# Optimization experiments

Hardware: AMD Instinct MI355X
Metric: run time of the kernel (lower is better)

## Reference

```python
import jax, jax.numpy as jnp
import numpy as np

HID, H, D, DFF = 128, 4, 128, 2048   # hidden_dim, nheads, out_feats per head, dim_feedforward
N, E, B = 32768, 524288, 32
EPS = 1e-5
SLOPE = 0.2  # DGL EdgeGATConv negative_slope default


def setup_inputs() -> dict:
    key = jax.random.key(0)
    ks = jax.random.split(key, 16)
    s = 0.05
    return {
        "h": jax.random.normal(ks[0], (N, HID), jnp.float32),
        "e": jax.random.normal(ks[1], (E, 1), jnp.float32),
        "src": jax.random.randint(ks[2], (E,), 0, N, jnp.int32),
        "dst": jax.random.randint(ks[3], (E,), 0, N, jnp.int32),
        "batch_size": B,
        # EdgeGATConv params (fc / fc_edge / res_fc are bias-free in DGL)
        "W_fc": jax.random.normal(ks[4], (HID, H * D), jnp.float32) * s,
        "attn_l": jax.random.normal(ks[5], (H, D), jnp.float32) * s,
        "attn_r": jax.random.normal(ks[6], (H, D), jnp.float32) * s,
        "W_fe": jax.random.normal(ks[7], (1, H * D), jnp.float32) * s,
        "attn_e": jax.random.normal(ks[8], (H, D), jnp.float32) * s,
        "W_res": jax.random.normal(ks[9], (HID, H * D), jnp.float32) * s,
        "gat_bias": jnp.zeros((H * D,), jnp.float32),
        # linear_mha + norms + FFN
        "W_mha": jax.random.normal(ks[10], (H * D, HID), jnp.float32) * s,
        "b_mha": jnp.zeros((HID,), jnp.float32),
        "n1_g": jnp.ones((HID,), jnp.float32),
        "n1_b": jnp.zeros((HID,), jnp.float32),
        "n2_g": jnp.ones((HID,), jnp.float32),
        "n2_b": jnp.zeros((HID,), jnp.float32),
        "W1": jax.random.normal(ks[11], (HID, DFF), jnp.float32) * s,
        "b1": jnp.zeros((DFF,), jnp.float32),
        "W2": jax.random.normal(ks[12], (DFF, HID), jnp.float32) * s,
        "b2": jnp.zeros((HID,), jnp.float32),
    }


def _ln(x, g, b):
    mu = x.mean(-1, keepdims=True)
    var = ((x - mu) ** 2).mean(-1, keepdims=True)
    return (x - mu) * jax.lax.rsqrt(var + EPS) * g + b


def reference(h, e, src, dst, batch_size, W_fc, attn_l, attn_r, W_fe, attn_e,
              W_res, gat_bias, W_mha, b_mha, n1_g, n1_b, n2_g, n2_b,
              W1, b1, W2, b2):
    n = h.shape[0]
    h0 = h
    # --- EdgeGATConv (eval mode: dropouts are identity) ---
    ft = (h @ W_fc).reshape(n, H, D)                         # (N,H,D)
    el = jnp.einsum("nhd,hd->nh", ft, attn_l)                # (N,H)
    er = jnp.einsum("nhd,hd->nh", ft, attn_r)
    fe = (e @ W_fe).reshape(-1, H, D)                        # (E,H,D)
    ee = jnp.einsum("ehd,hd->eh", fe, attn_e)                # (E,H)
    sc = jax.nn.leaky_relu(el[src] + er[dst] + ee, SLOPE)    # (E,H)
    # segment softmax over incoming edges of each dst node
    m = jax.ops.segment_max(sc, dst, num_segments=n)         # (N,H)
    m = jnp.where(jnp.isfinite(m), m, 0.0)                   # empty segments
    w = jnp.exp(sc - m[dst])
    z = jax.ops.segment_sum(w, dst, num_segments=n)
    zd = z[dst]
    alpha = w / jnp.where(zd == 0, 1.0, zd)                  # (E,H)
    msg = ft[src] * alpha[:, :, None]                        # (E,H,D)
    rst = jax.ops.segment_sum(msg, dst, num_segments=n)      # (N,H,D)
    rst = rst + (h0 @ W_res).reshape(n, H, D) + gat_bias.reshape(1, H, D)
    # --- transformer wrapper ---
    x = jax.nn.relu(rst).reshape(n, H * D)
    x = jax.nn.relu(x @ W_mha + b_mha)
    x = _ln(h0 + x, n1_g, n1_b)
    x = x.reshape(batch_size, -1, x.shape[1])                # (B, N/B, HID)
    ff = jax.nn.relu(x @ W1 + b1) @ W2 + b2
    return _ln(x + ff, n2_g, n2_b)
```

## Files before the change

kernel.cpp:

```cpp
#include <hip/hip_runtime.h>
#include <hip/hip_bf16.h>

#define N_NODES 32768
#define E_EDGES 524288
#define HIDDIM 128
#define FDIM 512
#define DFF 2048
#define LN_EPS 1e-5f
#define SLOPE 0.2f
#define CAP 64

typedef __bf16 bf16_t;
typedef __bf16 bf16x8 __attribute__((ext_vector_type(8)));
typedef float f32x4 __attribute__((ext_vector_type(4)));
typedef float f32x2 __attribute__((ext_vector_type(2)));

#define GLD_LDS16(gp, lp) __builtin_amdgcn_global_load_lds( \
    (const __attribute__((address_space(1))) unsigned int*)(gp), \
    (__attribute__((address_space(3))) unsigned int*)(lp), 16, 0, 0)

__device__ inline unsigned char f32_to_e4m3(float v) {
#if __has_builtin(__builtin_amdgcn_cvt_pk_fp8_f32)
    return (unsigned char)(__builtin_amdgcn_cvt_pk_fp8_f32(v, v, 0, false) & 0xff);
#else
    unsigned bits = __float_as_uint(v);
    unsigned sign = (bits >> 24) & 0x80;
    float av = fabsf(v);
    if (av >= 448.f) return (unsigned char)(sign | 0x7E);
    int e = (int)((bits >> 23) & 0xFF) - 127;
    if (e < -6) { int n = (int)rintf(av * 512.f); return (unsigned char)(sign | n); }
    float ulp = exp2f((float)(e - 3));
    int n = (int)rintf(av / ulp);
    if (n == 16) { e += 1; n = 8; }
    return (unsigned char)(sign | ((e + 7) << 3) | (n - 8));
#endif
}
template<bool HI>
__device__ inline f32x2 e4m3x2_to_f32(unsigned u) {
#if __has_builtin(__builtin_amdgcn_cvt_pk_f32_fp8)
    return __builtin_amdgcn_cvt_pk_f32_fp8(u, HI);
#else
    f32x2 r;
    unsigned b0 = HI ? ((u >> 16) & 0xff) : (u & 0xff);
    unsigned b1 = HI ? ((u >> 24) & 0xff) : ((u >> 8) & 0xff);
    unsigned bs[2] = {b0, b1};
    for (int i = 0; i < 2; ++i) {
        unsigned b = bs[i];
        float s = (b & 0x80) ? -1.f : 1.f;
        int e = (b >> 3) & 15, m = b & 7;
        float v = e ? (8 + m) * exp2f((float)(e - 10)) : m * exp2f(-9.f);
        r[i] = s * v;
    }
    return r;
#endif
}

__global__ __launch_bounds__(256) void gemm_mfma(const bf16_t* __restrict__ A,
                                                 const bf16_t* __restrict__ Bp,
                                                 bf16_t* __restrict__ C,
                                                 int M, int N, int K) {
    __shared__ __align__(16) bf16_t lA[4096];
    __shared__ __align__(16) bf16_t lB[4096];
    const int tid = threadIdx.x;
    const int lane = tid & 63;
    const int wave = tid >> 6;
    const int wm = (wave >> 1) * 64, wn = (wave & 1) * 64;
    const int row0 = blockIdx.y * 128, col0 = blockIdx.x * 128;
    const int ko = lane >> 4;
    const int rl = lane & 15;
    f32x4 acc[4][4] = {};
    const int c0 = tid, c1 = tid + 256;
    const int g0 = c0 >> 7, m0 = c0 & 127;
    const int g1 = c1 >> 7, m1 = c1 & 127;
    for (int k0 = 0; k0 < K; k0 += 32) {
        __syncthreads();
        GLD_LDS16(A + (size_t)(row0 + m0) * K + k0 + g0 * 8, lA + c0 * 8);
        GLD_LDS16(A + (size_t)(row0 + m1) * K + k0 + g1 * 8, lA + c1 * 8);
        GLD_LDS16(Bp + ((size_t)(k0 / 8 + g0) * N + col0 + m0) * 8, lB + c0 * 8);
        GLD_LDS16(Bp + ((size_t)(k0 / 8 + g1) * N + col0 + m1) * 8, lB + c1 * 8);
        __syncthreads();
        bf16x8 af[4], bfr[4];
#pragma unroll
        for (int i = 0; i < 4; ++i) {
            af[i]  = *(const bf16x8*)&lA[(ko * 128 + wm + i * 16 + rl) * 8];
            bfr[i] = *(const bf16x8*)&lB[(ko * 128 + wn + i * 16 + rl) * 8];
        }
#pragma unroll
        for (int i = 0; i < 4; ++i)
#pragma unroll
            for (int j = 0; j < 4; ++j)
                acc[i][j] = __builtin_amdgcn_mfma_f32_16x16x32_bf16(af[i], bfr[j], acc[i][j], 0, 0, 0);
    }
    const int cr = (lane >> 4) * 4;
    const int cc = lane & 15;
#pragma unroll
    for (int i = 0; i < 4; ++i)
#pragma unroll
        for (int j = 0; j < 4; ++j) {
            const int col = col0 + wn + j * 16 + cc;
#pragma unroll
            for (int r = 0; r < 4; ++r) {
                const int row = row0 + wm + i * 16 + cr + r;
                C[(size_t)row * N + col] = (bf16_t)acc[i][j][r];
            }
        }
}

__global__ __launch_bounds__(256) void gemm_ft(const bf16_t* __restrict__ A,
                                               const bf16_t* __restrict__ Bp,
                                               const float* __restrict__ attn_l,
                                               const float* __restrict__ attn_r,
                                               unsigned char* __restrict__ ft8,
                                               float* __restrict__ el,
                                               float* __restrict__ er) {
    __shared__ __align__(16) bf16_t lA[4096];
    __shared__ __align__(16) bf16_t lB[4096];
    __shared__ float s_el[2][128], s_er[2][128];
    const int tid = threadIdx.x, lane = tid & 63, wave = tid >> 6;
    const int wm = (wave >> 1) * 64, wn = (wave & 1) * 64;
    const int row0 = blockIdx.y * 128;
    const int head = blockIdx.x, col0 = head * 128;
    const int ko = lane >> 4, rl = lane & 15;
    f32x4 acc[4][4] = {};
    const int c0 = tid, c1 = tid + 256;
    const int g0 = c0 >> 7, m0 = c0 & 127;
    const int g1 = c1 >> 7, m1 = c1 & 127;
    for (int k0 = 0; k0 < 128; k0 += 32) {
        __syncthreads();
        GLD_LDS16(A + (size_t)(row0 + m0) * 128 + k0 + g0 * 8, lA + c0 * 8);
        GLD_LDS16(A + (size_t)(row0 + m1) * 128 + k0 + g1 * 8, lA + c1 * 8);
        GLD_LDS16(Bp + ((size_t)(k0 / 8 + g0) * 512 + col0 + m0) * 8, lB + c0 * 8);
        GLD_LDS16(Bp + ((size_t)(k0 / 8 + g1) * 512 + col0 + m1) * 8, lB + c1 * 8);
        __syncthreads();
        bf16x8 af[4], bfr[4];
#pragma unroll
        for (int i = 0; i < 4; ++i) {
            af[i]  = *(const bf16x8*)&lA[(ko * 128 + wm + i * 16 + rl) * 8];
            bfr[i] = *(const bf16x8*)&lB[(ko * 128 + wn + i * 16 + rl) * 8];
        }
#pragma unroll
        for (int i = 0; i < 4; ++i)
#pragma unroll
            for (int j = 0; j < 4; ++j)
                acc[i][j] = __builtin_amdgcn_mfma_f32_16x16x32_bf16(af[i], bfr[j], acc[i][j], 0, 0, 0);
    }
    const int cr = (lane >> 4) * 4, cc = lane & 15;
    float al[4], ar[4];
#pragma unroll
    for (int j = 0; j < 4; ++j) {
        al[j] = attn_l[col0 + wn + j * 16 + cc];
        ar[j] = attn_r[col0 + wn + j * 16 + cc];
    }
#pragma unroll
    for (int i = 0; i < 4; ++i)
#pragma unroll
        for (int r = 0; r < 4; ++r) {
            const int row = row0 + wm + i * 16 + cr + r;
            float pel = 0.f, per = 0.f;
#pragma unroll
            for (int j = 0; j < 4; ++j) {
                const float v = acc[i][j][r];
                ft8[(size_t)row * 512 + col0 + wn + j * 16 + cc] = f32_to_e4m3(v);
                pel += v * al[j];
                per += v * ar[j];
            }
#pragma unroll
            for (int m = 1; m < 16; m <<= 1) {
                pel += __shfl_xor(pel, m);
                per += __shfl_xor(per, m);
            }
            if (cc == 0) {
                s_el[wn >> 6][wm + i * 16 + cr + r] = pel;
                s_er[wn >> 6][wm + i * 16 + cr + r] = per;
            }
        }
    __syncthreads();
    if (tid < 128) {
        el[(size_t)(row0 + tid) * 4 + head] = s_el[0][tid] + s_el[1][tid];
        er[(size_t)(row0 + tid) * 4 + head] = s_er[0][tid] + s_er[1][tid];
    }
}

__global__ __launch_bounds__(256) void gemm_mha_ln(const bf16_t* __restrict__ A,
                                                   const bf16_t* __restrict__ Bp,
                                                   const float* __restrict__ bias,
                                                   const float* __restrict__ h0,
                                                   const float* __restrict__ gamma,
                                                   const float* __restrict__ beta,
                                                   bf16_t* __restrict__ out) {
    __shared__ __align__(16) bf16_t lA[4096];
    __shared__ __align__(16) bf16_t lB[4096];
    __shared__ float s_s1[2][128], s_s2[2][128], s_mu[128], s_rs[128];
    const int tid = threadIdx.x, lane = tid & 63, wave = tid >> 6;
    const int wm = (wave >> 1) * 64, wn = (wave & 1) * 64;
    const int row0 = blockIdx.x * 128;
    const int ko = lane >> 4, rl = lane & 15;
    f32x4 acc[4][4] = {};
    const int c0 = tid, c1 = tid + 256;
    const int g0 = c0 >> 7, m0 = c0 & 127;
    const int g1 = c1 >> 7, m1 = c1 & 127;
    for (int k0 = 0; k0 < 512; k0 += 32) {
        __syncthreads();
        GLD_LDS16(A + (size_t)(row0 + m0) * 512 + k0 + g0 * 8, lA + c0 * 8);
        GLD_LDS16(A + (size_t)(row0 + m1) * 512 + k0 + g1 * 8, lA + c1 * 8);
        GLD_LDS16(Bp + ((size_t)(k0 / 8 + g0) * 128 + m0) * 8, lB + c0 * 8);
        GLD_LDS16(Bp + ((size_t)(k0 / 8 + g1) * 128 + m1) * 8, lB + c1 * 8);
        __syncthreads();
        bf16x8 af[4], bfr[4];
#pragma unroll
        for (int i = 0; i < 4; ++i) {
            af[i]  = *(const bf16x8*)&lA[(ko * 128 + wm + i * 16 + rl) * 8];
            bfr[i] = *(const bf16x8*)&lB[(ko * 128 + wn + i * 16 + rl) * 8];
        }
#pragma unroll
        for (int i = 0; i < 4; ++i)
#pragma unroll
            for (int j = 0; j < 4; ++j)
                acc[i][j] = __builtin_amdgcn_mfma_f32_16x16x32_bf16(af[i], bfr[j], acc[i][j], 0, 0, 0);
    }
    const int cr = (lane >> 4) * 4, cc = lane & 15;
#pragma unroll
    for (int j = 0; j < 4; ++j) {
        const int col = wn + j * 16 + cc;
        const float bb = bias[col];
#pragma unroll
        for (int i = 0; i < 4; ++i)
#pragma unroll
            for (int r = 0; r < 4; ++r) {
                const int row = row0 + wm + i * 16 + cr + r;
                acc[i][j][r] = fmaxf(acc[i][j][r] + bb, 0.f) + h0[(size_t)row * 128 + col];
            }
    }
#pragma unroll
    for (int i = 0; i < 4; ++i)
#pragma unroll
        for (int r = 0; r < 4; ++r) {
            float s1 = 0.f, s2 = 0.f;
#pragma unroll
            for (int j = 0; j < 4; ++j) { const float v = acc[i][j][r]; s1 += v; s2 += v * v; }
#pragma unroll
            for (int m = 1; m < 16; m <<= 1) {
                s1 += __shfl_xor(s1, m);
                s2 += __shfl_xor(s2, m);
            }
            if (cc == 0) {
                s_s1[wn >> 6][wm + i * 16 + cr + r] = s1;
                s_s2[wn >> 6][wm + i * 16 + cr + r] = s2;
            }
        }
    __syncthreads();
    if (tid < 128) {
        const float a = s_s1[0][tid] + s_s1[1][tid];
        const float q = s_s2[0][tid] + s_s2[1][tid];
        const float mu = a * (1.f / 128.f);
        s_mu[tid] = mu;
        s_rs[tid] = rsqrtf(q * (1.f / 128.f) - mu * mu + LN_EPS);
    }
    __syncthreads();
#pragma unroll
    for (int j = 0; j < 4; ++j) {
        const int col = wn + j * 16 + cc;
        const float gg = gamma[col], bb = beta[col];
#pragma unroll
        for (int i = 0; i < 4; ++i)
#pragma unroll
            for (int r = 0; r < 4; ++r) {
                const int rloc = wm + i * 16 + cr + r;
                out[(size_t)(row0 + rloc) * 128 + col] =
                    (bf16_t)((acc[i][j][r] - s_mu[rloc]) * s_rs[rloc] * gg + bb);
            }
    }
}

__global__ __launch_bounds__(256, 1) void ffn_fused(const bf16_t* __restrict__ x3,
                                                    const bf16_t* __restrict__ W1p,
                                                    const float* __restrict__ b1,
                                                    const bf16_t* __restrict__ W2p,
                                                    const float* __restrict__ b2,
                                                    const float* __restrict__ gamma,
                                                    const float* __restrict__ beta,
                                                    float* __restrict__ out) {
    __shared__ __align__(16) bf16_t lX[16384];
    __shared__ __align__(16) bf16_t lW1[16384];
    __shared__ __align__(16) bf16_t lW2[16384];
    __shared__ __align__(16) bf16_t lY[16384];
    __shared__ float s_s1[2][128], s_s2[2][128], s_mu[128], s_rs[128];
    const int tid = threadIdx.x, lane = tid & 63, wave = tid >> 6;
    const int wm = (wave >> 1) * 64, wn = (wave & 1) * 64;
    const int row0 = blockIdx.x * 128;
    const int ko = lane >> 4, rl = lane & 15;
    const int cr = (lane >> 4) * 4, cc = lane & 15;
#pragma unroll
    for (int it = 0; it < 8; ++it) {
        const int c = it * 256 + tid;
        const int g = c >> 7, m = c & 127;
        GLD_LDS16(x3 + (size_t)(row0 + m) * 128 + g * 8, lX + c * 8);
    }
    f32x4 xacc[4][4] = {};
    for (int ch = 0; ch < 16; ++ch) {
        __syncthreads();
#pragma unroll
        for (int it = 0; it < 8; ++it) {
            const int c = it * 256 + tid;
            const int g = c >> 7, n = c & 127;
            GLD_LDS16(W1p + ((size_t)g * 2048 + ch * 128 + n) * 8, lW1 + c * 8);
            GLD_LDS16(W2p + ((size_t)(ch * 16 + g) * 128 + n) * 8, lW2 + c * 8);
        }
        __syncthreads();
        f32x4 yacc[4][4] = {};
#pragma unroll
        for (int kk = 0; kk < 4; ++kk) {
            bf16x8 af[4], bfr[4];
#pragma unroll
            for (int i = 0; i < 4; ++i) {
                af[i]  = *(const bf16x8*)&lX[((kk * 4 + ko) * 128 + wm + i * 16 + rl) * 8];
                bfr[i] = *(const bf16x8*)&lW1[((kk * 4 + ko) * 128 + wn + i * 16 + rl) * 8];
            }
#pragma unroll
            for (int i = 0; i < 4; ++i)
#pragma unroll
                for (int j = 0; j < 4; ++j)
                    yacc[i][j] = __builtin_amdgcn_mfma_f32_16x16x32_bf16(af[i], bfr[j], yacc[i][j], 0, 0, 0);
        }
#pragma unroll
        for (int j = 0; j < 4; ++j) {
            const int col = wn + j * 16 + cc;
            const float bb = b1[ch * 128 + col];
#pragma unroll
            for (int i = 0; i < 4; ++i)
#pragma unroll
                for (int r = 0; r < 4; ++r) {
                    const float v = fmaxf(yacc[i][j][r] + bb, 0.f);
                    const int row = wm + i * 16 + cr + r;
                    lY[((col >> 3) * 128 + row) * 8 + (col & 7)] = (bf16_t)v;
                }
        }
        __syncthreads();
#pragma unroll
        for (int kk = 0; kk < 4; ++kk) {
            bf16x8 af[4], bfr[4];
#pragma unroll
            for (int i = 0; i < 4; ++i) {
                af[i]  = *(const bf16x8*)&lY[((kk * 4 + ko) * 128 + wm + i * 16 + rl) * 8];
                bfr[i] = *(const bf16x8*)&lW2[((kk * 4 + ko) * 128 + wn + i * 16 + rl) * 8];
            }
#pragma unroll
            for (int i = 0; i < 4; ++i)
#pragma unroll
                for (int j = 0; j < 4; ++j)
                    xacc[i][j] = __builtin_amdgcn_mfma_f32_16x16x32_bf16(af[i], bfr[j], xacc[i][j], 0, 0, 0);
        }
    }
#pragma unroll
    for (int j = 0; j < 4; ++j) {
        const int col = wn + j * 16 + cc;
        const float bb = b2[col];
#pragma unroll
        for (int i = 0; i < 4; ++i)
#pragma unroll
            for (int r = 0; r < 4; ++r) {
                const int row = wm + i * 16 + cr + r;
                const float x3v = (float)lX[((col >> 3) * 128 + row) * 8 + (col & 7)];
                xacc[i][j][r] += bb + x3v;
            }
    }
#pragma unroll
    for (int i = 0; i < 4; ++i)
#pragma unroll
        for (int r = 0; r < 4; ++r) {
            float s1 = 0.f, s2 = 0.f;
#pragma unroll
            for (int j = 0; j < 4; ++j) { const float v = xacc[i][j][r]; s1 += v; s2 += v * v; }
#pragma unroll
            for (int m = 1; m < 16; m <<= 1) {
                s1 += __shfl_xor(s1, m);
                s2 += __shfl_xor(s2, m);
            }
            if (cc == 0) {
                s_s1[wn >> 6][wm + i * 16 + cr + r] = s1;
                s_s2[wn >> 6][wm + i * 16 + cr + r] = s2;
            }
        }
    __syncthreads();
    if (tid < 128) {
        const float a = s_s1[0][tid] + s_s1[1][tid];
        const float q = s_s2[0][tid] + s_s2[1][tid];
        const float mu = a * (1.f / 128.f);
        s_mu[tid] = mu;
        s_rs[tid] = rsqrtf(q * (1.f / 128.f) - mu * mu + LN_EPS);
    }
    __syncthreads();
#pragma unroll
    for (int j = 0; j < 4; ++j) {
        const int col = wn + j * 16 + cc;
        const float gg = gamma[col], bb = beta[col];
#pragma unroll
        for (int i = 0; i < 4; ++i)
#pragma unroll
            for (int r = 0; r < 4; ++r) {
                const int rloc = wm + i * 16 + cr + r;
                out[(size_t)(row0 + rloc) * 128 + col] =
                    (xacc[i][j][r] - s_mu[rloc]) * s_rs[rloc] * gg + bb;
            }
    }
}

__global__ __launch_bounds__(256) void pack_b(const float* __restrict__ B, bf16_t* __restrict__ out,
                                              int K8, int N) {
    const int id = blockIdx.x * 256 + threadIdx.x;
    if (id >= K8 * N) return;
    const int g = id / N, n = id % N;
    union { bf16_t b[8]; uint4 u; } pk;
#pragma unroll
    for (int j = 0; j < 8; ++j) pk.b[j] = (bf16_t)B[(size_t)(g * 8 + j) * N + n];
    *(uint4*)(out + (size_t)id * 8) = pk.u;
}

__global__ __launch_bounds__(256) void f2b_kernel(const float* __restrict__ x, bf16_t* __restrict__ o) {
    const int id = blockIdx.x * 256 + threadIdx.x;
    const float4 v = ((const float4*)x)[id];
    union { bf16_t b[4]; uint2 u; } pk;
    pk.b[0] = (bf16_t)v.x; pk.b[1] = (bf16_t)v.y; pk.b[2] = (bf16_t)v.z; pk.b[3] = (bf16_t)v.w;
    *(uint2*)(o + (size_t)id * 4) = pk.u;
}

__global__ __launch_bounds__(128) void ce_kernel(const float* __restrict__ W_fe,
                                                 const float* __restrict__ attn_e,
                                                 float* __restrict__ ce) {
    const int t = threadIdx.x;
    const float4 w = ((const float4*)W_fe)[t];
    const float4 a = ((const float4*)attn_e)[t];
    float p = w.x * a.x + w.y * a.y + w.z * a.z + w.w * a.w;
    for (int off = 16; off; off >>= 1) p += __shfl_down(p, off, 32);
    if ((t & 31) == 0) ce[t >> 5] = p;
}

__global__ __launch_bounds__(256) void edge_build(const float* __restrict__ evals,
                                                  const int* __restrict__ src,
                                                  const int* __restrict__ dst,
                                                  const float* __restrict__ el,
                                                  const float* __restrict__ er,
                                                  const float* __restrict__ ce,
                                                  int* __restrict__ cursor,
                                                  int* __restrict__ csr_src,
                                                  float4* __restrict__ csr_w) {
    const int e = blockIdx.x * 256 + threadIdx.x;
    const int s = src[e], d = dst[e];
    const float ev = evals[e];
    const float4 l = *(const float4*)(el + (size_t)s * 4);
    const float4 r = *(const float4*)(er + (size_t)d * 4);
    const float4 c = *(const float4*)ce;
    float4 w;
    {
        float v;
        v = l.x + r.x + ev * c.x; v = v >= 0.f ? v : SLOPE * v; w.x = expf(v);
        v = l.y + r.y + ev * c.y; v = v >= 0.f ? v : SLOPE * v; w.y = expf(v);
        v = l.z + r.z + ev * c.z; v = v >= 0.f ? v : SLOPE * v; w.z = expf(v);
        v = l.w + r.w + ev * c.w; v = v >= 0.f ? v : SLOPE * v; w.w = expf(v);
    }
    const int pos = atomicAdd(&cursor[d], 1);
    if (pos < CAP) {
        csr_src[(size_t)d * CAP + pos] = s;
        csr_w[(size_t)d * CAP + pos] = w;
    }
}

__global__ __launch_bounds__(128) void aggregate_kernel(const unsigned char* __restrict__ ft8,
                                                        const bf16_t* __restrict__ res,
                                                        const int* __restrict__ cursor,
                                                        const int* __restrict__ csr_src,
                                                        const float4* __restrict__ csr_w,
                                                        const float* __restrict__ gat_bias,
                                                        bf16_t* __restrict__ x1) {
    const int n = blockIdx.x, t = threadIdx.x;
    __shared__ int s_src[CAP];
    __shared__ float s_w[CAP][4];
    const int deg = min(cursor[n], CAP);
    const int ht = t >> 5;
    if (t < deg) {
        s_src[t] = csr_src[(size_t)n * CAP + t];
        *(float4*)s_w[t] = csr_w[(size_t)n * CAP + t];
    }
    __syncthreads();
    float4 acc = {0.f, 0.f, 0.f, 0.f};
    float z = 0.f;
    for (int j = 0; j < deg; ++j) {
        const float w = s_w[j][ht];
        z += w;
        const unsigned u = *(const unsigned*)(ft8 + (size_t)s_src[j] * 512 + t * 4);
        const f32x2 lo = e4m3x2_to_f32<false>(u);
        const f32x2 hi = e4m3x2_to_f32<true>(u);
        acc.x += w * lo[0]; acc.y += w * lo[1];
        acc.z += w * hi[0]; acc.w += w * hi[1];
    }
    const float rz = deg > 0 ? 1.f / z : 0.f;
    const uint2 ur = *(const uint2*)(res + (size_t)n * FDIM + t * 4);
    const float4 gb = ((const float4*)gat_bias)[t];
    union { bf16_t b[4]; uint2 u; } pk;
    pk.b[0] = (bf16_t)fmaxf(acc.x * rz + __uint_as_float(ur.x << 16) + gb.x, 0.f);
    pk.b[1] = (bf16_t)fmaxf(acc.y * rz + __uint_as_float(ur.x & 0xFFFF0000u) + gb.y, 0.f);
    pk.b[2] = (bf16_t)fmaxf(acc.z * rz + __uint_as_float(ur.y << 16) + gb.z, 0.f);
    pk.b[3] = (bf16_t)fmaxf(acc.w * rz + __uint_as_float(ur.y & 0xFFFF0000u) + gb.w, 0.f);
    *(uint2*)(x1 + (size_t)n * FDIM + t * 4) = pk.u;
}

extern "C" void kernel_launch(void* const* d_in, const int* in_sizes, int n_in,
                              void* d_out, int out_size, void* d_ws, size_t ws_size,
                              hipStream_t stream) {
    const float* h        = (const float*)d_in[0];
    const float* evals    = (const float*)d_in[1];
    const int*   src      = (const int*)d_in[2];
    const int*   dst      = (const int*)d_in[3];
    const float* W_fc     = (const float*)d_in[5];
    const float* attn_l   = (const float*)d_in[6];
    const float* attn_r   = (const float*)d_in[7];
    const float* W_fe     = (const float*)d_in[8];
    const float* attn_e   = (const float*)d_in[9];
    const float* W_res    = (const float*)d_in[10];
    const float* gat_bias = (const float*)d_in[11];
    const float* W_mha    = (const float*)d_in[12];
    const float* b_mha    = (const float*)d_in[13];
    const float* n1_g     = (const float*)d_in[14];
    const float* n1_b     = (const float*)d_in[15];
    const float* n2_g     = (const float*)d_in[16];
    const float* n2_b     = (const float*)d_in[17];
    const float* W1       = (const float*)d_in[18];
    const float* b1       = (const float*)d_in[19];
    const float* W2       = (const float*)d_in[20];
    const float* b2       = (const float*)d_in[21];

    char* ws = (char*)d_ws;
    unsigned char* ft8 = (unsigned char*)(ws + 0);
    bf16_t* res     = (bf16_t*)(ws + 16777216ull);
    bf16_t* x1      = (bf16_t*)(ws + 50331648ull);
    float4* csr_w   = (float4*)(ws + 83886080ull);
    int*    csr_src = (int*)   (ws + 117440512ull);
    bf16_t* x3b     = (bf16_t*)(ws + 125829120ull);
    bf16_t* hb      = (bf16_t*)(ws + 134217728ull);
    bf16_t* Wfc_p   = (bf16_t*)(ws + 142606336ull);
    bf16_t* Wres_p  = (bf16_t*)(ws + 142737408ull);
    bf16_t* Wmha_p  = (bf16_t*)(ws + 142868480ull);
    bf16_t* W1_p    = (bf16_t*)(ws + 142999552ull);
    bf16_t* W2_p    = (bf16_t*)(ws + 143523840ull);
    float*  el      = (float*) (ws + 144048128ull);
    float*  er      = (float*) (ws + 144572416ull);
    float*  ce      = (float*) (ws + 145096704ull);
    int*    cursor  = (int*)   (ws + 145096768ull);

    if (ws_size < 146000000ull) return;

    (void)hipMemsetAsync(cursor, 0, 131072, stream);

    f2b_kernel<<<4096, 256, 0, stream>>>(h, hb);
    pack_b<<<32, 256, 0, stream>>>(W_fc, Wfc_p, 16, 512);
    pack_b<<<32, 256, 0, stream>>>(W_res, Wres_p, 16, 512);
    pack_b<<<32, 256, 0, stream>>>(W_mha, Wmha_p, 64, 128);
    pack_b<<<128, 256, 0, stream>>>(W1, W1_p, 16, 2048);
    pack_b<<<128, 256, 0, stream>>>(W2, W2_p, 256, 128);
    ce_kernel<<<1, 128, 0, stream>>>(W_fe, attn_e, ce);

    gemm_ft<<<dim3(4, 256), 256, 0, stream>>>(hb, Wfc_p, attn_l, attn_r, ft8, el, er);
    gemm_mfma<<<dim3(4, 256), 256, 0, stream>>>(hb, Wres_p, res, N_NODES, FDIM, 128);
    edge_build<<<E_EDGES / 256, 256, 0, stream>>>(evals, src, dst, el, er, ce, cursor, csr_src, csr_w);
    aggregate_kernel<<<N_NODES, 128, 0, stream>>>(ft8, res, cursor, csr_src, csr_w, gat_bias, x1);
    gemm_mha_ln<<<256, 256, 0, stream>>>(x1, Wmha_p, b_mha, h, n1_g, n1_b, x3b);
    ffn_fused<<<256, 256, 0, stream>>>(x3b, W1_p, b1, W2_p, b2, n2_g, n2_b, (float*)d_out);
}
```

Before: 315.8 us.

## Double-buffer FFN weight chunks, merge prep kernels, use fast exp

The fused FFN kernel now processes DFF in 32 chunks of 64 with double-buffered W1/W2 tiles in LDS. The next chunk's loads are issued during the second GEMM, and the X fragments are kept in registers across all chunks. This aims to hide global-to-LDS latency and cut one barrier per chunk, at the cost of more register pressure and smaller per-chunk MFMA work. Separately, seven small prep launches (bf16 cast, weight packing, edge-attention constant) are merged into one kernel, and edge_build uses __expf instead of expf.

Result: slower. 328.7 us (+4.1%).

```diff
diff --git a/kernel.cpp b/kernel.cpp
--- a/kernel.cpp
+++ b/kernel.cpp
@@ -53,6 +53,52 @@
     }
     return r;
 #endif
+}
+
+__device__ inline void pack_range(const float* __restrict__ B, bf16_t* __restrict__ out,
+                                  int id, int N) {
+    const int g = id / N, n = id % N;
+    union { bf16_t b[8]; uint4 u; } pk;
+#pragma unroll
+    for (int j = 0; j < 8; ++j) pk.b[j] = (bf16_t)B[(size_t)(g * 8 + j) * N + n];
+    *(uint4*)(out + (size_t)id * 8) = pk.u;
+}
+
+__global__ __launch_bounds__(256) void prep_kernel(const float* __restrict__ h, bf16_t* __restrict__ hb,
+                                                   const float* __restrict__ W_fc, bf16_t* __restrict__ Wfc_p,
+                                                   const float* __restrict__ W_res, bf16_t* __restrict__ Wres_p,
+                                                   const float* __restrict__ W_mha, bf16_t* __restrict__ Wmha_p,
+                                                   const float* __restrict__ W1, bf16_t* __restrict__ W1_p,
+                                                   const float* __restrict__ W2, bf16_t* __restrict__ W2_p,
+                                                   const float* __restrict__ W_fe, const float* __restrict__ attn_e,
+                                                   float* __restrict__ ce) {
+    int bid = blockIdx.x;
+    const int tid = threadIdx.x;
+    if (bid < 4096) {
+        const int id = bid * 256 + tid;
+        const float4 v = ((const float4*)h)[id];
+        union { bf16_t b[4]; uint2 u; } pk;
+        pk.b[0] = (bf16_t)v.x; pk.b[1] = (bf16_t)v.y; pk.b[2] = (bf16_t)v.z; pk.b[3] = (bf16_t)v.w;
+        *(uint2*)(hb + (size_t)id * 4) = pk.u;
+        return;
+    }
+    bid -= 4096;
+    if (bid < 32)  { pack_range(W_fc,  Wfc_p,  bid * 256 + tid, 512);  return; }
+    bid -= 32;
+    if (bid < 32)  { pack_range(W_res, Wres_p, bid * 256 + tid, 512);  return; }
+    bid -= 32;
+    if (bid < 32)  { pack_range(W_mha, Wmha_p, bid * 256 + tid, 128);  return; }
+    bid -= 32;
+    if (bid < 128) { pack_range(W1,    W1_p,   bid * 256 + tid, 2048); return; }
+    bid -= 128;
+    if (bid < 128) { pack_range(W2,    W2_p,   bid * 256 + tid, 128);  return; }
+    if (tid < 128) {
+        const float4 w = ((const float4*)W_fe)[tid];
+        const float4 a = ((const float4*)attn_e)[tid];
+        float p = w.x * a.x + w.y * a.y + w.z * a.z + w.w * a.w;
+        for (int off = 16; off; off >>= 1) p += __shfl_down(p, off, 32);
+        if ((tid & 31) == 0) ce[tid >> 5] = p;
+    }
 }
 
 __global__ __launch_bounds__(256) void gemm_mfma(const bf16_t* __restrict__ A,
@@ -281,86 +327,101 @@
                                                     const float* __restrict__ beta,
                                                     float* __restrict__ out) {
     __shared__ __align__(16) bf16_t lX[16384];
-    __shared__ __align__(16) bf16_t lW1[16384];
-    __shared__ __align__(16) bf16_t lW2[16384];
-    __shared__ __align__(16) bf16_t lY[16384];
+    __shared__ __align__(16) bf16_t lW1[2][8192];
+    __shared__ __align__(16) bf16_t lW2[2][8192];
+    __shared__ __align__(16) bf16_t lY[8192];
     __shared__ float s_s1[2][128], s_s2[2][128], s_mu[128], s_rs[128];
     const int tid = threadIdx.x, lane = tid & 63, wave = tid >> 6;
-    const int wm = (wave >> 1) * 64, wn = (wave & 1) * 64;
+    const int wm = (wave >> 1) * 64;
+    const int wn1 = (wave & 1) * 32;
+    const int wn2 = (wave & 1) * 64;
     const int row0 = blockIdx.x * 128;
     const int ko = lane >> 4, rl = lane & 15;
-    const int cr = (lane >> 4) * 4, cc = lane & 15;
+    const int cr = ko * 4, cc = rl;
+
 #pragma unroll
     for (int it = 0; it < 8; ++it) {
+        const int c = it * 256 + tid, g = c >> 7, m = c & 127;
+        GLD_LDS16(x3 + (size_t)(row0 + m) * 128 + g * 8, lX + c * 8);
+    }
+#pragma unroll
+    for (int it = 0; it < 4; ++it) {
         const int c = it * 256 + tid;
-        const int g = c >> 7, m = c & 127;
-        GLD_LDS16(x3 + (size_t)(row0 + m) * 128 + g * 8, lX + c * 8);
-    }
+        { const int g = c >> 6, n = c & 63;  GLD_LDS16(W1p + ((size_t)g * 2048 + n) * 8, lW1[0] + c * 8); }
+        { const int g = c >> 7, n = c & 127; GLD_LDS16(W2p + ((size_t)g * 128 + n) * 8, lW2[0] + c * 8); }
+    }
+    __syncthreads();
+    bf16x8 afx[4][4];
+#pragma unroll
+    for (int i = 0; i < 4; ++i)
+#pragma unroll
+        for (int kk = 0; kk < 4; ++kk)
+            afx[i][kk] = *(const bf16x8*)&lX[((kk * 4 + ko) * 128 + wm + i * 16 + rl) * 8];
+
     f32x4 xacc[4][4] = {};
-    for (int ch = 0; ch < 16; ++ch) {
-        __syncthreads();
-#pragma unroll
-        for (int it = 0; it < 8; ++it) {
-            const int c = it * 256 + tid;
-            const int g = c >> 7, n = c & 127;
-            GLD_LDS16(W1p + ((size_t)g * 2048 + ch * 128 + n) * 8, lW1 + c * 8);
-            GLD_LDS16(W2p + ((size_t)(ch * 16 + g) * 128 + n) * 8, lW2 + c * 8);
-        }
-        __syncthreads();
-        f32x4 yacc[4][4] = {};
+    for (int ch = 0; ch < 32; ++ch) {
+        const int b = ch & 1;
+        f32x4 yacc[4][2] = {};
 #pragma unroll
         for (int kk = 0; kk < 4; ++kk) {
-            bf16x8 af[4], bfr[4];
-#pragma unroll
-            for (int i = 0; i < 4; ++i) {
-                af[i]  = *(const bf16x8*)&lX[((kk * 4 + ko) * 128 + wm + i * 16 + rl) * 8];
-                bfr[i] = *(const bf16x8*)&lW1[((kk * 4 + ko) * 128 + wn + i * 16 + rl) * 8];
-            }
+            bf16x8 bfr[2];
+#pragma unroll
+            for (int j = 0; j < 2; ++j)
+                bfr[j] = *(const bf16x8*)&lW1[b][((kk * 4 + ko) * 64 + wn1 + j * 16 + rl) * 8];
 #pragma unroll
             for (int i = 0; i < 4; ++i)
 #pragma unroll
+                for (int j = 0; j < 2; ++j)
+                    yacc[i][j] = __builtin_amdgcn_mfma_f32_16x16x32_bf16(afx[i][kk], bfr[j], yacc[i][j], 0, 0, 0);
+        }
+#pragma unroll
+        for (int j = 0; j < 2; ++j) {
+            const int dff = wn1 + j * 16 + cc;
+            const float bb = b1[ch * 64 + dff];
+#pragma unroll
+            for (int i = 0; i < 4; ++i)
+#pragma unroll
+                for (int r = 0; r < 4; ++r)
+                    lY[((dff >> 3) * 128 + wm + i * 16 + cr + r) * 8 + (dff & 7)] =
+                        (bf16_t)fmaxf(yacc[i][j][r] + bb, 0.f);
+        }
+        __syncthreads();
+        if (ch + 1 < 32) {
+            const int nb = b ^ 1, nch = ch + 1;
+#pragma unroll
+            for (int it = 0; it < 4; ++it) {
+                const int c = it * 256 + tid;
+                { const int g = c >> 6, n = c & 63;  GLD_LDS16(W1p + ((size_t)g * 2048 + nch * 64 + n) * 8, lW1[nb] + c * 8); }
+                { const int g = c >> 7, n = c & 127; GLD_LDS16(W2p + ((size_t)(nch * 8 + g) * 128 + n) * 8, lW2[nb] + c * 8); }
+            }
+        }
+#pragma unroll
+        for (int kk = 0; kk < 2; ++kk) {
+            bf16x8 afY[4], bfr2[4];
+#pragma unroll
+            for (int i = 0; i < 4; ++i)
+                afY[i] = *(const bf16x8*)&lY[((kk * 4 + ko) * 128 + wm + i * 16 + rl) * 8];
+#pragma unroll
+            for (int j = 0; j < 4; ++j)
+                bfr2[j] = *(const bf16x8*)&lW2[b][((kk * 4 + ko) * 128 + wn2 + j * 16 + rl) * 8];
+#pragma unroll
+            for (int i = 0; i < 4; ++i)
+#pragma unroll
                 for (int j = 0; j < 4; ++j)
-                    yacc[i][j] = __builtin_amdgcn_mfma_f32_16x16x32_bf16(af[i], bfr[j], yacc[i][j], 0, 0, 0);
-        }
-#pragma unroll
-        for (int j = 0; j < 4; ++j) {
-            const int col = wn + j * 16 + cc;
-            const float bb = b1[ch * 128 + col];
-#pragma unroll
-            for (int i = 0; i < 4; ++i)
-#pragma unroll
-                for (int r = 0; r < 4; ++r) {
-                    const float v = fmaxf(yacc[i][j][r] + bb, 0.f);
-                    const int row = wm + i * 16 + cr + r;
-                    lY[((col >> 3) * 128 + row) * 8 + (col & 7)] = (bf16_t)v;
-                }
-        }
-        __syncthreads();
-#pragma unroll
-        for (int kk = 0; kk < 4; ++kk) {
-            bf16x8 af[4], bfr[4];
-#pragma unroll
-            for (int i = 0; i < 4; ++i) {
-                af[i]  = *(const bf16x8*)&lY[((kk * 4 + ko) * 128 + wm + i * 16 + rl) * 8];
-                bfr[i] = *(const bf16x8*)&lW2[((kk * 4 + ko) * 128 + wn + i * 16 + rl) * 8];
-            }
-#pragma unroll
-            for (int i = 0; i < 4; ++i)
-#pragma unroll
-                for (int j = 0; j < 4; ++j)
-                    xacc[i][j] = __builtin_amdgcn_mfma_f32_16x16x32_bf16(af[i], bfr[j], xacc[i][j], 0, 0, 0);
-        }
+                    xacc[i][j] = __builtin_amdgcn_mfma_f32_16x16x32_bf16(afY[i], bfr2[j], xacc[i][j], 0, 0, 0);
+        }
+        __syncthreads();
     }
 #pragma unroll
     for (int j = 0; j < 4; ++j) {
-        const int col = wn + j * 16 + cc;
+        const int col = wn2 + j * 16 + cc;
         const float bb = b2[col];
 #pragma unroll
         for (int i = 0; i < 4; ++i)
 #pragma unroll
             for (int r = 0; r < 4; ++r) {
-                const int row = wm + i * 16 + cr + r;
-                const float x3v = (float)lX[((col >> 3) * 128 + row) * 8 + (col & 7)];
+                const int rloc = wm + i * 16 + cr + r;
+                const float x3v = (float)lX[((col >> 3) * 128 + rloc) * 8 + (col & 7)];
                 xacc[i][j][r] += bb + x3v;
             }
     }
@@ -377,8 +438,8 @@
                 s2 += __shfl_xor(s2, m);
             }
             if (cc == 0) {
-                s_s1[wn >> 6][wm + i * 16 + cr + r] = s1;
-                s_s2[wn >> 6][wm + i * 16 + cr + r] = s2;
+                s_s1[wn2 >> 6][wm + i * 16 + cr + r] = s1;
+                s_s2[wn2 >> 6][wm + i * 16 + cr + r] = s2;
             }
         }
     __syncthreads();
@@ -392,7 +453,7 @@
     __syncthreads();
 #pragma unroll
     for (int j = 0; j < 4; ++j) {
-        const int col = wn + j * 16 + cc;
+        const int col = wn2 + j * 16 + cc;
         const float gg = gamma[col], bb = beta[col];
 #pragma unroll
         for (int i = 0; i < 4; ++i)
@@ -403,36 +464,6 @@
                     (xacc[i][j][r] - s_mu[rloc]) * s_rs[rloc] * gg + bb;
             }
     }
-}
-
-__global__ __launch_bounds__(256) void pack_b(const float* __restrict__ B, bf16_t* __restrict__ out,
-                                              int K8, int N) {
-    const int id = blockIdx.x * 256 + threadIdx.x;
-    if (id >= K8 * N) return;
-    const int g = id / N, n = id % N;
-    union { bf16_t b[8]; uint4 u; } pk;
-#pragma unroll
-    for (int j = 0; j < 8; ++j) pk.b[j] = (bf16_t)B[(size_t)(g * 8 + j) * N + n];
-    *(uint4*)(out + (size_t)id * 8) = pk.u;
-}
-
-__global__ __launch_bounds__(256) void f2b_kernel(const float* __restrict__ x, bf16_t* __restrict__ o) {
-    const int id = blockIdx.x * 256 + threadIdx.x;
-    const float4 v = ((const float4*)x)[id];
-    union { bf16_t b[4]; uint2 u; } pk;
-    pk.b[0] = (bf16_t)v.x; pk.b[1] = (bf16_t)v.y; pk.b[2] = (bf16_t)v.z; pk.b[3] = (bf16_t)v.w;
-    *(uint2*)(o + (size_t)id * 4) = pk.u;
-}
-
-__global__ __launch_bounds__(128) void ce_kernel(const float* __restrict__ W_fe,
-                                                 const float* __restrict__ attn_e,
-                                                 float* __restrict__ ce) {
-    const int t = threadIdx.x;
-    const float4 w = ((const float4*)W_fe)[t];
-    const float4 a = ((const float4*)attn_e)[t];
-    float p = w.x * a.x + w.y * a.y + w.z * a.z + w.w * a.w;
-    for (int off = 16; off; off >>= 1) p += __shfl_down(p, off, 32);
-    if ((t & 31) == 0) ce[t >> 5] = p;
 }
 
 __global__ __launch_bounds__(256) void edge_build(const float* __restrict__ evals,
@@ -453,10 +484,10 @@
     float4 w;
     {
         float v;
-        v = l.x + r.x + ev * c.x; v = v >= 0.f ? v : SLOPE * v; w.x = expf(v);
-        v = l.y + r.y + ev * c.y; v = v >= 0.f ? v : SLOPE * v; w.y = expf(v);
-        v = l.z + r.z + ev * c.z; v = v >= 0.f ? v : SLOPE * v; w.z = expf(v);
-        v = l.w + r.w + ev * c.w; v = v >= 0.f ? v : SLOPE * v; w.w = expf(v);
+        v = l.x + r.x + ev * c.x; v = v >= 0.f ? v : SLOPE * v; w.x = __expf(v);
+        v = l.y + r.y + ev * c.y; v = v >= 0.f ? v : SLOPE * v; w.y = __expf(v);
+        v = l.z + r.z + ev * c.z; v = v >= 0.f ? v : SLOPE * v; w.z = __expf(v);
+        v = l.w + r.w + ev * c.w; v = v >= 0.f ? v : SLOPE * v; w.w = __expf(v);
     }
     const int pos = atomicAdd(&cursor[d], 1);
     if (pos < CAP) {
@@ -551,14 +582,9 @@
 
     (void)hipMemsetAsync(cursor, 0, 131072, stream);
 
-    f2b_kernel<<<4096, 256, 0, stream>>>(h, hb);
-    pack_b<<<32, 256, 0, stream>>>(W_fc, Wfc_p, 16, 512);
-    pack_b<<<32, 256, 0, stream>>>(W_res, Wres_p, 16, 512);
-    pack_b<<<32, 256, 0, stream>>>(W_mha, Wmha_p, 64, 128);
-    pack_b<<<128, 256, 0, stream>>>(W1, W1_p, 16, 2048);
-    pack_b<<<128, 256, 0, stream>>>(W2, W2_p, 256, 128);
-    ce_kernel<<<1, 128, 0, stream>>>(W_fe, attn_e, ce);
-
+    prep_kernel<<<4449, 256, 0, stream>>>(h, hb, W_fc, Wfc_p, W_res, Wres_p,
+                                          W_mha, Wmha_p, W1, W1_p, W2, W2_p,
+                                          W_fe, attn_e, ce);
     gemm_ft<<<dim3(4, 256), 256, 0, stream>>>(hb, Wfc_p, attn_l, attn_r, ft8, el, er);
     gemm_mfma<<<dim3(4, 256), 256, 0, stream>>>(hb, Wres_p, res, N_NODES, FDIM, 128);
     edge_build<<<E_EDGES / 256, 256, 0, stream>>>(evals, src, dst, el, er, ce, cursor, csr_src, csr_w);
```
